# Kernel tuning notes

Hardware: AMD Instinct MI355X
Metric: run time of the kernel (lower is better)

## Reference

```python
import jax, jax.numpy as jnp
import numpy as np

NB, NA, NC, NH, NW = 64, 3, 13, 76, 76
NL = 12                     # num_labels per ground-truth row
NET_W = NET_H = 608.0       # net_width / net_height
MAX_T, NVALID = 50, 20      # GT slots per image / number of valid GTs
ANCHORS = np.array([[0.70, 1.18], [1.26, 2.10], [2.64, 4.20]], dtype=np.float32)
BETA = 2.8 / 100.0          # huber beta
EPS = 1e-12
IGNORE_THRESH = 0.5


def iou_cxcywh(b1, b2):
    # boxes [..., 4] in (cx, cy, w, h); matches multi_bbox_ious(x1y1x2y2=False)
    x1, y1, w1, h1 = b1[..., 0], b1[..., 1], b1[..., 2], b1[..., 3]
    x2, y2, w2, h2 = b2[..., 0], b2[..., 1], b2[..., 2], b2[..., 3]
    cw = jnp.minimum(x1 + 0.5 * w1, x2 + 0.5 * w2) - jnp.maximum(x1 - 0.5 * w1, x2 - 0.5 * w2)
    ch = jnp.minimum(y1 + 0.5 * h1, y2 + 0.5 * h2) - jnp.maximum(y1 - 0.5 * h1, y2 - 0.5 * h2)
    inter = jnp.where((cw > 0) & (ch > 0), cw * ch, 0.0)
    return inter / (w1 * h1 + w2 * h2 - inter)


def _bce(p, t):
    # elementwise binary cross entropy with safe logs (torch clamps log, same effect)
    return -(t * jnp.log(jnp.clip(p, EPS, 1.0)) + (1.0 - t) * jnp.log(jnp.clip(1.0 - p, EPS, 1.0)))


def setup_inputs() -> dict:
    key = jax.random.key(0)
    k1, k2, k3, k4, k5 = jax.random.split(key, 5)
    output = jax.random.normal(k1, (NB, NA * (NL + NC), NH, NW), dtype=jnp.float32)
    cls_id = jax.random.randint(k2, (NB, MAX_T), 0, NC).astype(jnp.float32)
    xy = jax.random.uniform(k3, (NB, MAX_T, 2), minval=0.05, maxval=0.95)
    extra = jax.random.uniform(k4, (NB, MAX_T, 7), minval=-0.5, maxval=0.5)
    wh = jax.random.uniform(k5, (NB, MAX_T, 2), minval=0.05, maxval=0.30)
    tbox = jnp.concatenate([cls_id[..., None], xy, extra, wh], axis=-1)  # (NB, 50, 12)
    vmask = (jnp.arange(MAX_T) < NVALID)[None, :, None].astype(jnp.float32)
    target = (tbox * vmask).reshape(NB, MAX_T * NL)  # rows after NVALID are all-zero (break)
    return {"output": output, "target": target, "anchors": jnp.asarray(ANCHORS)}


def _yolo_loss(output, target, anchors):
    target = jax.lax.stop_gradient(target)  # torch: target.detach()
    nB, nA, nC, nH, nW = NB, NA, NC, NH, NW
    nAnchors, nPixels = nA * nH * nW, nH * nW
    cad = nB * nAnchors

    out5 = output.reshape(nB, nA, NL + nC, nH, nW)
    coord = out5[:, :, : NL - 1].reshape(nB * nA, NL - 1, nPixels)
    coord = coord.transpose(1, 0, 2).reshape(NL - 1, cad)          # (11, cad), flat order b,a,h,w
    coord = jnp.concatenate([jax.nn.sigmoid(coord[:2]), coord[2:]], axis=0)
    conf = jax.nn.sigmoid(out5[:, :, NL - 1].reshape(cad))
    cls_logits = out5[:, :, NL:].reshape(nB * nA, nC, nPixels).transpose(0, 2, 1).reshape(cad, nC)

    grid_x = jnp.broadcast_to(jnp.arange(nW, dtype=jnp.float32), (nB * nA, nH, nW)).reshape(cad)
    grid_y = jnp.broadcast_to(jnp.arange(nH, dtype=jnp.float32)[:, None], (nB * nA, nH, nW)).reshape(cad)
    anchor_w = jnp.broadcast_to(anchors[None, :, 0, None], (nB, nA, nPixels)).reshape(cad)
    anchor_h = jnp.broadcast_to(anchors[None, :, 1, None], (nB, nA, nPixels)).reshape(cad)
    pb = jnp.concatenate([
        (coord[0] + grid_x)[None], (coord[1] + grid_y)[None],
        coord[2:9],
        (jnp.exp(coord[9]) * anchor_w)[None], (jnp.exp(coord[10]) * anchor_h)[None],
    ], axis=0)                                                     # (11, cad)
    pred_boxes = jax.lax.stop_gradient(pb.T)                       # detached, as in torch

    # ---- build_targets, vectorized over batch and GT boxes ----
    tbox = target.reshape(nB, MAX_T, NL)
    # emulate the data-dependent `break` at first row with x == 0
    valid = jnp.cumprod((tbox[:, :, 1] > 0).astype(jnp.int32), axis=1).astype(bool)  # (nB,50)
    gx, gy = tbox[:, :, 1] * nW, tbox[:, :, 2] * nH
    gw, gh = tbox[:, :, 10] * NET_W, tbox[:, :, 11] * NET_H

    box_cols = jnp.array([0, 1, 9, 10])
    pbb = pred_boxes.reshape(nB, nAnchors, NL - 1)[:, :, box_cols]  # (nB, nAnchors, 4)
    gtb = jnp.stack([gx, gy, gw, gh], axis=-1)                      # (nB, 50, 4)
    ious_all = iou_cxcywh(pbb[:, None], gtb[:, :, None])            # (nB, 50, nAnchors)
    cur_ious = jnp.where(valid[:, :, None], ious_all, 0.0).max(axis=1)
    noobj = jnp.where(cur_ious > IGNORE_THRESH, 0.0, 1.0).reshape(cad)

    # best anchor by wh IoU at origin
    aw, ah = anchors[:, 0], anchors[:, 1]
    inter = jnp.minimum(gw[..., None], aw) * jnp.minimum(gh[..., None], ah)
    best_n = jnp.argmax(inter / (gw[..., None] * gh[..., None] + aw * ah - inter), axis=-1)  # (nB,50)

    gi = jnp.clip(jnp.floor(gx).astype(jnp.int32), 0, nW - 1)
    gj = jnp.clip(jnp.floor(gy).astype(jnp.int32), 0, nH - 1)
    flat = jnp.arange(nB)[:, None] * nAnchors + best_n * nPixels + gj * nW + gi  # (nB,50)
    pred_sel = pred_boxes[flat.reshape(-1)][:, box_cols].reshape(nB, MAX_T, 4)
    iou_t = iou_cxcywh(gtb, pred_sel)                                # (nB,50)
    idx = jnp.where(valid, flat, cad).reshape(-1)                    # invalid GTs -> dummy slot cad

    aw_b, ah_b = aw[best_n], ah[best_n]
    sgw = jnp.where(valid, gw, 1.0)
    sgh = jnp.where(valid, gh, 1.0)
    vals = jnp.stack([gx - gi.astype(jnp.float32), gy - gj.astype(jnp.float32),
                      tbox[:, :, 3], tbox[:, :, 4], tbox[:, :, 5], tbox[:, :, 6],
                      tbox[:, :, 7], tbox[:, :, 8], tbox[:, :, 9],
                      jnp.log(sgw / aw_b), jnp.log(sgh / ah_b)], axis=-1)  # (nB,50,11)

    obj = jnp.zeros(cad + 1).at[idx].set(1.0)[:cad]
    noobj = jnp.concatenate([noobj, jnp.zeros(1)]).at[idx].set(0.0)[:cad]
    tcoord = jnp.zeros((cad + 1, NL - 1)).at[idx].set(vals.reshape(-1, NL - 1))[:cad].T  # (11,cad)
    tconf = jnp.zeros(cad + 1).at[idx].set(iou_t.reshape(-1))[:cad]   # rescore == 1
    cls_t = tbox[:, :, 0].astype(jnp.int32).reshape(-1)
    tcls = jnp.zeros((cad + 1, nC)).at[idx, cls_t].set(1.0)[:cad]

    # ---- losses: masked sums are equivalent to torch boolean-index-then-sum ----
    m = obj  # (cad,) float {0,1}
    loss_coord = (_bce(coord[0:2], tcoord[0:2]) * m).sum() / nB \
               + (((coord[9:11] - tcoord[9:11]) ** 2) * m).sum() / nB

    diff = (coord[2:5] - tcoord[2:5]) * m                             # (3, cad)
    dis = jnp.sqrt((diff ** 2).sum(axis=1))                           # per-channel L2, as in huber_loss
    in_w = (dis <= BETA).astype(jnp.float32)
    loss_trans = ((0.5 * diff ** 2 / BETA).sum(axis=1) * in_w
                  + (jnp.abs(diff).sum(axis=1) - BETA / 2) * (1.0 - in_w)).sum() / nB

    rot = coord[5:9]
    rot_n = rot / jnp.maximum(jnp.sqrt((rot ** 2).sum(axis=0, keepdims=True)), 1e-12)  # F.normalize dim=0
    loss_rot = (jnp.abs(rot_n - tcoord[5:9]) * m).sum() / nB

    conf_mask = obj + noobj
    loss_conf = _bce(conf * conf_mask, tconf * conf_mask).sum() / nB

    x = cls_logits
    bce_cls = jnp.maximum(x, 0.0) - x * tcls + jnp.log1p(jnp.exp(-jnp.abs(x)))  # BCEWithLogits
    loss_cls = (bce_cls * m[:, None]).sum() / nB

    return loss_coord + loss_trans + loss_rot + loss_conf + loss_cls


def reference(output, target, anchors):
    return _yolo_loss(output, target, anchors)
```

## Files before the change

kernel.cpp:

```cpp
#include <hip/hip_runtime.h>
#include <math.h>

#define NBATCH 64
#define NANCH_PER 3
#define NCLS 13
#define NH 76
#define NW 76
#define NPIX (NH*NW)
#define MAXT 50
#define NLC 12
#define NCH (NLC + NCLS)
#define BETA_C 0.028f
#define EPS_C 1e-12f
#define NET_WH 608.0f
#define CHUNKS 23
#define NBLK (NBATCH*NANCH_PER*CHUNKS)
#define LOGEPS 27.6310211159285f

struct TRec {
  float x1, x2, y1, y2;
  float area;
  int   flat;
  float iou;
  int   cls;
  float vals[11];
  float pad;
};

__device__ __forceinline__ float sigmoidf_(float x) { return 1.0f / (1.0f + __expf(-x)); }

__device__ __forceinline__ float bcef_(float p, float t) {
  float lp = __logf(fminf(fmaxf(p, EPS_C), 1.0f));
  float lq = __logf(fminf(fmaxf(1.0f - p, EPS_C), 1.0f));
  return -(t * lp + (1.0f - t) * lq);
}

__global__ void yolo_prep(const float* __restrict__ outp,
                          const float* __restrict__ target,
                          const float* __restrict__ anchors,
                          TRec* __restrict__ recs,
                          int* __restrict__ nvalid,
                          float* __restrict__ minarr)
{
  int b = blockIdx.x;
  int t = threadIdx.x;
  const float* tb = target + b * (MAXT * NLC) + t * NLC;
  float v1 = (t < MAXT) ? tb[1] : 0.0f;
  unsigned long long vm = __ballot(v1 > 0.0f);
  bool valid = false;
  float marea = 1e30f;
  if (t < MAXT) {
    valid = ((~vm) & ((2ULL << t) - 1ULL)) == 0ULL;

    float gx = tb[1] * (float)NW, gy = tb[2] * (float)NH;
    float gw = tb[10] * NET_WH,   gh = tb[11] * NET_WH;

    int bn = 0; float best = -1e30f;
    for (int k = 0; k < NANCH_PER; ++k) {
      float aw = anchors[2*k], ah = anchors[2*k+1];
      float inter = fminf(gw, aw) * fminf(gh, ah);
      float r = inter / (gw * gh + aw * ah - inter);
      if (r > best) { best = r; bn = k; }
    }
    float aw = anchors[2*bn], ah = anchors[2*bn+1];

    int gi = min(max((int)floorf(gx), 0), NW - 1);
    int gj = min(max((int)floorf(gy), 0), NH - 1);
    int pixq = gj * NW + gi;
    int flat = bn * NPIX + pixq;

    const float* cb = outp + ((size_t)(b * NANCH_PER + bn) * NCH) * NPIX + pixq;
    float px = sigmoidf_(cb[0]) + (float)gi;
    float py = sigmoidf_(cb[NPIX]) + (float)gj;
    float pw = __expf(cb[9 * NPIX]) * aw;
    float ph = __expf(cb[10 * NPIX]) * ah;

    float cw  = fminf(gx + 0.5f*gw, px + 0.5f*pw) - fmaxf(gx - 0.5f*gw, px - 0.5f*pw);
    float chh = fminf(gy + 0.5f*gh, py + 0.5f*ph) - fmaxf(gy - 0.5f*gh, py - 0.5f*ph);
    float inter = (cw > 0.0f && chh > 0.0f) ? cw * chh : 0.0f;
    float iou = inter / (gw * gh + pw * ph - inter);

    TRec r;
    r.x1 = gx - 0.5f * gw; r.x2 = gx + 0.5f * gw;
    r.y1 = gy - 0.5f * gh; r.y2 = gy + 0.5f * gh;
    r.area = gw * gh;
    r.flat = valid ? flat : -1;
    r.iou = iou;
    r.cls = (int)tb[0];
    r.vals[0] = gx - (float)gi;
    r.vals[1] = gy - (float)gj;
    #pragma unroll
    for (int k = 0; k < 7; ++k) r.vals[2 + k] = tb[3 + k];
    float sgw = valid ? gw : 1.0f, sgh = valid ? gh : 1.0f;
    r.vals[9]  = __logf(sgw / aw);
    r.vals[10] = __logf(sgh / ah);
    r.pad = 0.0f;
    recs[b * MAXT + t] = r;
    if (valid) marea = gw * gh;
  }
  unsigned long long vm2 = __ballot(valid);
  #pragma unroll
  for (int off = 32; off > 0; off >>= 1) marea = fminf(marea, __shfl_xor(marea, off, 64));
  if (t == 0) { nvalid[b] = __popcll(vm2); minarr[b] = marea; }
}

__global__ __launch_bounds__(256) void yolo_loss(
    const float* __restrict__ outp,
    const TRec* __restrict__ recs,
    const int* __restrict__ nvalid,
    const float* __restrict__ minarr,
    const float* __restrict__ anchors,
    float* __restrict__ partial)
{
  __shared__ float srec[MAXT * 20];
  __shared__ int s_nv;
  __shared__ float s_minarea;
  __shared__ unsigned long long s_mmask;
  __shared__ float wsum[4];

  int blk = blockIdx.x;
  int b   = blk / (NANCH_PER * CHUNKS);
  int rem = blk % (NANCH_PER * CHUNKS);
  int a   = rem / CHUNKS;
  int c0  = (rem % CHUNKS) * 256;
  int pix = c0 + threadIdx.x;

  const float* src = (const float*)(recs + b * MAXT);
  for (int k = threadIdx.x; k < MAXT * 20; k += 256) srec[k] = src[k];
  if (threadIdx.x == 0) { s_nv = nvalid[b]; s_minarea = minarr[b]; }
  __syncthreads();
  const TRec* R = (const TRec*)srec;

  if (threadIdx.x < 64) {
    int t = threadIdx.x;
    int lo = a * NPIX + c0, hi = lo + 256;
    bool in = (t < MAXT) && (t < s_nv);
    int f = in ? R[t].flat : -1;
    unsigned long long mm = __ballot(in && f >= lo && f < hi);
    if (t == 0) s_mmask = mm;
  }
  __syncthreads();

  float local = 0.0f;
  if (pix < NPIX) {
    const float* cb = outp + ((size_t)(b * NANCH_PER + a) * NCH) * NPIX + pix;
    float tw = cb[9 * NPIX];
    float th = cb[10 * NPIX];
    float tc = cb[11 * NPIX];
    float aw = anchors[2*a], ah = anchors[2*a+1];
    float parea = __expf(tw + th) * aw * ah;
    int myflat = a * NPIX + pix;

    int match = -1;
    unsigned cmask = 0;
    unsigned long long mm = s_mmask;
    while (mm) {
      int t = (int)__builtin_ctzll(mm); mm &= mm - 1;
      if (R[t].flat == myflat) { match = t; cmask |= (1u << R[t].cls); }
    }

    bool over = false;
    if (match < 0 && 2.0f * parea > s_minarea) {
      int j = pix / NW;
      int i = pix - j * NW;
      float sx = sigmoidf_(cb[0]), sy = sigmoidf_(cb[NPIX]);
      float pw = __expf(tw) * aw, ph = __expf(th) * ah;
      float px = sx + (float)i, py = sy + (float)j;
      float pxl = px - 0.5f * pw, pxh = px + 0.5f * pw;
      float pyl = py - 0.5f * ph, pyh = py + 0.5f * ph;
      int nv = s_nv;
      for (int t = 0; t < nv; ++t) {
        float x1 = R[t].x1, x2 = R[t].x2, y1 = R[t].y1, y2 = R[t].y2;
        float ta = R[t].area;
        float cw  = fminf(pxh, x2) - fmaxf(pxl, x1);
        float chh = fminf(pyh, y2) - fmaxf(pyl, y1);
        float inter = (cw > 0.0f && chh > 0.0f) ? cw * chh : 0.0f;
        over = over || (3.0f * inter > parea + ta);
      }
    }

    if (match >= 0) {
      int j = pix / NW;
      int i = pix - j * NW;
      float sx = sigmoidf_(cb[0]), sy = sigmoidf_(cb[NPIX]);
      float conf = sigmoidf_(tc);
      const TRec& r = R[match];
      local += bcef_(conf, r.iou);
      local += bcef_(sx, r.vals[0]) + bcef_(sy, r.vals[1]);
      float d9 = tw - r.vals[9], d10 = th - r.vals[10];
      local += d9 * d9 + d10 * d10;
      float c2 = cb[2 * NPIX], c3 = cb[3 * NPIX], c4 = cb[4 * NPIX];
      float e2 = c2 - r.vals[2], e3 = c3 - r.vals[3], e4 = c4 - r.vals[4];
      float ss = e2*e2 + e3*e3 + e4*e4;
      float dis = sqrtf(ss);
      if (dis <= BETA_C) local += 0.5f * ss / BETA_C;
      else local += fabsf(e2) + fabsf(e3) + fabsf(e4) - 0.5f * BETA_C;
      float c5 = cb[5 * NPIX], c6 = cb[6 * NPIX], c7 = cb[7 * NPIX], c8 = cb[8 * NPIX];
      float rn = fmaxf(sqrtf(c5*c5 + c6*c6 + c7*c7 + c8*c8), 1e-12f);
      local += fabsf(c5 / rn - r.vals[5]) + fabsf(c6 / rn - r.vals[6])
             + fabsf(c7 / rn - r.vals[7]) + fabsf(c8 / rn - r.vals[8]);
      #pragma unroll
      for (int c = 0; c < NCLS; ++c) {
        float x = cb[(NLC + c) * NPIX];
        float tt = ((cmask >> c) & 1u) ? 1.0f : 0.0f;
        local += fmaxf(x, 0.0f) - x * tt + __logf(1.0f + __expf(-fabsf(x)));
      }
    } else if (!over) {
      float e = __expf(tc);
      local += fminf(__logf(1.0f + e), LOGEPS);
    }
  }

  #pragma unroll
  for (int off = 32; off > 0; off >>= 1) local += __shfl_down(local, off, 64);
  if ((threadIdx.x & 63) == 0) wsum[threadIdx.x >> 6] = local;
  __syncthreads();
  if (threadIdx.x == 0) partial[blk] = wsum[0] + wsum[1] + wsum[2] + wsum[3];
}

__global__ __launch_bounds__(256) void yolo_final(const float* __restrict__ partial,
                                                  float* __restrict__ out)
{
  __shared__ float w[4];
  float s = 0.0f;
  for (int i = threadIdx.x; i < NBLK; i += 256) s += partial[i];
  #pragma unroll
  for (int off = 32; off > 0; off >>= 1) s += __shfl_down(s, off, 64);
  if ((threadIdx.x & 63) == 0) w[threadIdx.x >> 6] = s;
  __syncthreads();
  if (threadIdx.x == 0) out[0] = (w[0] + w[1] + w[2] + w[3]) * (1.0f / (float)NBATCH);
}

extern "C" void kernel_launch(void* const* d_in, const int* in_sizes, int n_in,
                              void* d_out, int out_size, void* d_ws, size_t ws_size,
                              hipStream_t stream) {
  const float* outp    = (const float*)d_in[0];
  const float* target  = (const float*)d_in[1];
  const float* anchors = (const float*)d_in[2];

  char* ws = (char*)d_ws;
  TRec*  recs    = (TRec*)ws;
  int*   nv      = (int*)(ws + 256000);
  float* minarr  = (float*)(ws + 256000 + 256);
  float* partial = (float*)(ws + 256000 + 512);

  yolo_prep<<<NBATCH, 64, 0, stream>>>(outp, target, anchors, recs, nv, minarr);
  yolo_loss<<<NBLK, 256, 0, stream>>>(outp, recs, nv, minarr, anchors, partial);
  yolo_final<<<1, 256, 0, stream>>>(partial, (float*)d_out);
}
```

Baseline: 161.0 us.

## Vectorize pixel loads with float4 and shrink grid to three sub-blocks per plane

The loss kernel now handles four pixels per thread through float4 loads of the tw/th/tc planes. Each block covers 2048 pixels in two 1024-pixel chunks, which cuts the grid from 23 chunks to 3 sub-blocks per (batch, anchor). GT data is split into SoA arrays (bounds float4, area, flat, cls), so only small fields are staged in shared memory and full records are fetched from global only on a match. The area threshold test is turned into a log-domain comparison so exp is skipped for rejected pixels. The smaller grid lowers occupancy and per-thread parallelism in exchange for wider loads and less staging overhead per block.

```diff
diff --git a/kernel.cpp b/kernel.cpp
--- a/kernel.cpp
+++ b/kernel.cpp
@@ -7,14 +7,15 @@
 #define NH 76
 #define NW 76
 #define NPIX (NH*NW)
+#define NG4 (NPIX/4)
 #define MAXT 50
 #define NLC 12
 #define NCH (NLC + NCLS)
 #define BETA_C 0.028f
 #define EPS_C 1e-12f
 #define NET_WH 608.0f
-#define CHUNKS 23
-#define NBLK (NBATCH*NANCH_PER*CHUNKS)
+#define SUBB 3
+#define NBLK (NBATCH*NANCH_PER*SUBB)
 #define LOGEPS 27.6310211159285f
 
 struct TRec {
@@ -39,6 +40,10 @@
                           const float* __restrict__ target,
                           const float* __restrict__ anchors,
                           TRec* __restrict__ recs,
+                          float4* __restrict__ boundsA,
+                          float* __restrict__ areaA,
+                          int* __restrict__ flatA,
+                          int* __restrict__ clsA,
                           int* __restrict__ nvalid,
                           float* __restrict__ minarr)
 {
@@ -96,6 +101,10 @@
     r.vals[10] = __logf(sgh / ah);
     r.pad = 0.0f;
     recs[b * MAXT + t] = r;
+    boundsA[b * MAXT + t] = make_float4(r.x1, r.x2, r.y1, r.y2);
+    areaA[b * MAXT + t] = r.area;
+    flatA[b * MAXT + t] = r.flat;
+    clsA[b * MAXT + t]  = r.cls;
     if (valid) marea = gw * gh;
   }
   unsigned long long vm2 = __ballot(valid);
@@ -104,118 +113,152 @@
   if (t == 0) { nvalid[b] = __popcll(vm2); minarr[b] = marea; }
 }
 
+__device__ __forceinline__ float elem4(const float4& v, int e) {
+  return e == 0 ? v.x : (e == 1 ? v.y : (e == 2 ? v.z : v.w));
+}
+
 __global__ __launch_bounds__(256) void yolo_loss(
     const float* __restrict__ outp,
     const TRec* __restrict__ recs,
+    const float4* __restrict__ boundsA,
+    const float* __restrict__ areaA,
+    const int* __restrict__ flatA,
+    const int* __restrict__ clsA,
     const int* __restrict__ nvalid,
     const float* __restrict__ minarr,
     const float* __restrict__ anchors,
     float* __restrict__ partial)
 {
-  __shared__ float srec[MAXT * 20];
-  __shared__ int s_nv;
-  __shared__ float s_minarea;
-  __shared__ unsigned long long s_mmask;
-  __shared__ float wsum[4];
+  __shared__ float4 s_b4[MAXT];
+  __shared__ float  s_area[MAXT];
+  __shared__ int    s_flat[MAXT];
+  __shared__ int    s_cls[MAXT];
+  __shared__ int    s_nv;
+  __shared__ float  s_minarea;
+  __shared__ unsigned long long s_mask[2];
+  __shared__ float  wsum[4];
 
   int blk = blockIdx.x;
-  int b   = blk / (NANCH_PER * CHUNKS);
-  int rem = blk % (NANCH_PER * CHUNKS);
-  int a   = rem / CHUNKS;
-  int c0  = (rem % CHUNKS) * 256;
-  int pix = c0 + threadIdx.x;
-
-  const float* src = (const float*)(recs + b * MAXT);
-  for (int k = threadIdx.x; k < MAXT * 20; k += 256) srec[k] = src[k];
-  if (threadIdx.x == 0) { s_nv = nvalid[b]; s_minarea = minarr[b]; }
+  int b   = blk / (NANCH_PER * SUBB);
+  int rem = blk % (NANCH_PER * SUBB);
+  int a   = rem / SUBB;
+  int sb  = rem % SUBB;
+  int tid = threadIdx.x;
+  int k0  = 2 * sb;
+
+  if (tid < MAXT) {
+    s_b4[tid]   = boundsA[b * MAXT + tid];
+    s_area[tid] = areaA[b * MAXT + tid];
+    s_flat[tid] = flatA[b * MAXT + tid];
+    s_cls[tid]  = clsA[b * MAXT + tid];
+  }
+  if (tid == 0) { s_nv = nvalid[b]; s_minarea = minarr[b]; }
   __syncthreads();
-  const TRec* R = (const TRec*)srec;
-
-  if (threadIdx.x < 64) {
-    int t = threadIdx.x;
-    int lo = a * NPIX + c0, hi = lo + 256;
-    bool in = (t < MAXT) && (t < s_nv);
-    int f = in ? R[t].flat : -1;
-    unsigned long long mm = __ballot(in && f >= lo && f < hi);
-    if (t == 0) s_mmask = mm;
+
+  if (tid < 64) {
+    int t = tid;
+    bool in = (t < s_nv);
+    int f = in ? s_flat[t] : -1;
+    #pragma unroll
+    for (int q = 0; q < 2; ++q) {
+      int lo = a * NPIX + (k0 + q) * 1024;
+      int hi = a * NPIX + min((k0 + q + 1) * 1024, NPIX);
+      unsigned long long mm = __ballot(in && f >= lo && f < hi);
+      if (t == 0) s_mask[q] = mm;
+    }
   }
   __syncthreads();
 
+  float aw = anchors[2*a], ah = anchors[2*a+1];
+  float logthr = __logf(s_minarea / (2.0f * aw * ah));
+
+  const float* plane = outp + ((size_t)(b * NANCH_PER + a) * NCH) * NPIX;
+  const float4* tw4p = (const float4*)(plane + 9  * NPIX);
+  const float4* th4p = (const float4*)(plane + 10 * NPIX);
+  const float4* tc4p = (const float4*)(plane + 11 * NPIX);
+
   float local = 0.0f;
-  if (pix < NPIX) {
-    const float* cb = outp + ((size_t)(b * NANCH_PER + a) * NCH) * NPIX + pix;
-    float tw = cb[9 * NPIX];
-    float th = cb[10 * NPIX];
-    float tc = cb[11 * NPIX];
-    float aw = anchors[2*a], ah = anchors[2*a+1];
-    float parea = __expf(tw + th) * aw * ah;
-    int myflat = a * NPIX + pix;
-
-    int match = -1;
-    unsigned cmask = 0;
-    unsigned long long mm = s_mmask;
-    while (mm) {
-      int t = (int)__builtin_ctzll(mm); mm &= mm - 1;
-      if (R[t].flat == myflat) { match = t; cmask |= (1u << R[t].cls); }
-    }
-
-    bool over = false;
-    if (match < 0 && 2.0f * parea > s_minarea) {
-      int j = pix / NW;
-      int i = pix - j * NW;
-      float sx = sigmoidf_(cb[0]), sy = sigmoidf_(cb[NPIX]);
-      float pw = __expf(tw) * aw, ph = __expf(th) * ah;
-      float px = sx + (float)i, py = sy + (float)j;
-      float pxl = px - 0.5f * pw, pxh = px + 0.5f * pw;
-      float pyl = py - 0.5f * ph, pyh = py + 0.5f * ph;
-      int nv = s_nv;
-      for (int t = 0; t < nv; ++t) {
-        float x1 = R[t].x1, x2 = R[t].x2, y1 = R[t].y1, y2 = R[t].y2;
-        float ta = R[t].area;
-        float cw  = fminf(pxh, x2) - fmaxf(pxl, x1);
-        float chh = fminf(pyh, y2) - fmaxf(pyl, y1);
-        float inter = (cw > 0.0f && chh > 0.0f) ? cw * chh : 0.0f;
-        over = over || (3.0f * inter > parea + ta);
+  #pragma unroll
+  for (int q = 0; q < 2; ++q) {
+    int g = (k0 + q) * 256 + tid;
+    if (g < NG4) {
+      float4 tw4 = tw4p[g];
+      float4 th4 = th4p[g];
+      float4 tc4 = tc4p[g];
+      unsigned long long mm0 = s_mask[q];
+      #pragma unroll
+      for (int e = 0; e < 4; ++e) {
+        float tw = elem4(tw4, e), th = elem4(th4, e), tc = elem4(tc4, e);
+        int pix = 4 * g + e;
+        int myflat = a * NPIX + pix;
+
+        int match = -1;
+        unsigned cmask = 0;
+        unsigned long long mm = mm0;
+        while (mm) {
+          int t = (int)__builtin_ctzll(mm); mm &= mm - 1;
+          if (s_flat[t] == myflat) { match = t; cmask |= (1u << s_cls[t]); }
+        }
+
+        bool over = false;
+        if (match < 0 && tw + th > logthr) {
+          int j = pix / NW;
+          int i = pix - j * NW;
+          float sx = sigmoidf_(plane[pix]), sy = sigmoidf_(plane[NPIX + pix]);
+          float pw = __expf(tw) * aw, ph = __expf(th) * ah;
+          float parea = pw * ph;
+          float px = sx + (float)i, py = sy + (float)j;
+          float pxl = px - 0.5f * pw, pxh = px + 0.5f * pw;
+          float pyl = py - 0.5f * ph, pyh = py + 0.5f * ph;
+          int nv = s_nv;
+          for (int t = 0; t < nv; ++t) {
+            float4 bb = s_b4[t];
+            float cw  = fminf(pxh, bb.y) - fmaxf(pxl, bb.x);
+            float chh = fminf(pyh, bb.w) - fmaxf(pyl, bb.z);
+            float inter = (cw > 0.0f && chh > 0.0f) ? cw * chh : 0.0f;
+            over = over || (3.0f * inter > parea + s_area[t]);
+          }
+        }
+
+        if (match >= 0) {
+          int j = pix / NW;
+          int i = pix - j * NW;
+          float sx = sigmoidf_(plane[pix]), sy = sigmoidf_(plane[NPIX + pix]);
+          float conf = sigmoidf_(tc);
+          TRec r = recs[b * MAXT + match];
+          local += bcef_(conf, r.iou);
+          local += bcef_(sx, r.vals[0]) + bcef_(sy, r.vals[1]);
+          float d9 = tw - r.vals[9], d10 = th - r.vals[10];
+          local += d9 * d9 + d10 * d10;
+          float c2 = plane[2*NPIX+pix], c3 = plane[3*NPIX+pix], c4 = plane[4*NPIX+pix];
+          float e2 = c2 - r.vals[2], e3 = c3 - r.vals[3], e4 = c4 - r.vals[4];
+          float ss = e2*e2 + e3*e3 + e4*e4;
+          float dis = sqrtf(ss);
+          if (dis <= BETA_C) local += 0.5f * ss / BETA_C;
+          else local += fabsf(e2) + fabsf(e3) + fabsf(e4) - 0.5f * BETA_C;
+          float c5 = plane[5*NPIX+pix], c6 = plane[6*NPIX+pix];
+          float c7 = plane[7*NPIX+pix], c8 = plane[8*NPIX+pix];
+          float rn = fmaxf(sqrtf(c5*c5 + c6*c6 + c7*c7 + c8*c8), 1e-12f);
+          local += fabsf(c5/rn - r.vals[5]) + fabsf(c6/rn - r.vals[6])
+                 + fabsf(c7/rn - r.vals[7]) + fabsf(c8/rn - r.vals[8]);
+          #pragma unroll
+          for (int c = 0; c < NCLS; ++c) {
+            float x = plane[(NLC + c) * NPIX + pix];
+            float tt = ((cmask >> c) & 1u) ? 1.0f : 0.0f;
+            local += fmaxf(x, 0.0f) - x * tt + __logf(1.0f + __expf(-fabsf(x)));
+          }
+        } else if (!over) {
+          local += fminf(__logf(1.0f + __expf(tc)), LOGEPS);
+        }
       }
     }
-
-    if (match >= 0) {
-      int j = pix / NW;
-      int i = pix - j * NW;
-      float sx = sigmoidf_(cb[0]), sy = sigmoidf_(cb[NPIX]);
-      float conf = sigmoidf_(tc);
-      const TRec& r = R[match];
-      local += bcef_(conf, r.iou);
-      local += bcef_(sx, r.vals[0]) + bcef_(sy, r.vals[1]);
-      float d9 = tw - r.vals[9], d10 = th - r.vals[10];
-      local += d9 * d9 + d10 * d10;
-      float c2 = cb[2 * NPIX], c3 = cb[3 * NPIX], c4 = cb[4 * NPIX];
-      float e2 = c2 - r.vals[2], e3 = c3 - r.vals[3], e4 = c4 - r.vals[4];
-      float ss = e2*e2 + e3*e3 + e4*e4;
-      float dis = sqrtf(ss);
-      if (dis <= BETA_C) local += 0.5f * ss / BETA_C;
-      else local += fabsf(e2) + fabsf(e3) + fabsf(e4) - 0.5f * BETA_C;
-      float c5 = cb[5 * NPIX], c6 = cb[6 * NPIX], c7 = cb[7 * NPIX], c8 = cb[8 * NPIX];
-      float rn = fmaxf(sqrtf(c5*c5 + c6*c6 + c7*c7 + c8*c8), 1e-12f);
-      local += fabsf(c5 / rn - r.vals[5]) + fabsf(c6 / rn - r.vals[6])
-             + fabsf(c7 / rn - r.vals[7]) + fabsf(c8 / rn - r.vals[8]);
-      #pragma unroll
-      for (int c = 0; c < NCLS; ++c) {
-        float x = cb[(NLC + c) * NPIX];
-        float tt = ((cmask >> c) & 1u) ? 1.0f : 0.0f;
-        local += fmaxf(x, 0.0f) - x * tt + __logf(1.0f + __expf(-fabsf(x)));
-      }
-    } else if (!over) {
-      float e = __expf(tc);
-      local += fminf(__logf(1.0f + e), LOGEPS);
-    }
   }
 
   #pragma unroll
   for (int off = 32; off > 0; off >>= 1) local += __shfl_down(local, off, 64);
-  if ((threadIdx.x & 63) == 0) wsum[threadIdx.x >> 6] = local;
+  if ((tid & 63) == 0) wsum[tid >> 6] = local;
   __syncthreads();
-  if (threadIdx.x == 0) partial[blk] = wsum[0] + wsum[1] + wsum[2] + wsum[3];
+  if (tid == 0) partial[blk] = wsum[0] + wsum[1] + wsum[2] + wsum[3];
 }
 
 __global__ __launch_bounds__(256) void yolo_final(const float* __restrict__ partial,
@@ -239,12 +282,19 @@
   const float* anchors = (const float*)d_in[2];
 
   char* ws = (char*)d_ws;
-  TRec*  recs    = (TRec*)ws;
-  int*   nv      = (int*)(ws + 256000);
-  float* minarr  = (float*)(ws + 256000 + 256);
-  float* partial = (float*)(ws + 256000 + 512);
-
-  yolo_prep<<<NBATCH, 64, 0, stream>>>(outp, target, anchors, recs, nv, minarr);
-  yolo_loss<<<NBLK, 256, 0, stream>>>(outp, recs, nv, minarr, anchors, partial);
+  size_t off = 0;
+  TRec*   recs    = (TRec*)  (ws + off); off += (size_t)NBATCH * MAXT * sizeof(TRec);
+  float4* boundsA = (float4*)(ws + off); off += (size_t)NBATCH * MAXT * sizeof(float4);
+  float*  areaA   = (float*) (ws + off); off += (size_t)NBATCH * MAXT * sizeof(float);
+  int*    flatA   = (int*)   (ws + off); off += (size_t)NBATCH * MAXT * sizeof(int);
+  int*    clsA    = (int*)   (ws + off); off += (size_t)NBATCH * MAXT * sizeof(int);
+  int*    nv      = (int*)   (ws + off); off += 256;
+  float*  minarr  = (float*) (ws + off); off += 256;
+  float*  partial = (float*) (ws + off);
+
+  yolo_prep<<<NBATCH, 64, 0, stream>>>(outp, target, anchors, recs, boundsA, areaA,
+                                       flatA, clsA, nv, minarr);
+  yolo_loss<<<NBLK, 256, 0, stream>>>(outp, recs, boundsA, areaA, flatA, clsA,
+                                      nv, minarr, anchors, partial);
   yolo_final<<<1, 256, 0, stream>>>(partial, (float*)d_out);
 }
```

Result: slower. 167.1 us (+3.8%).
